# Kernel optimization log

Measured on AMD Instinct MI355X. Metric: run time of the kernel, lower is better.

The kernel has to match this reference:

```python
import jax, jax.numpy as jnp
import numpy as np


def setup_inputs() -> dict:
    key = jax.random.key(0)
    ks = jax.random.split(key, 9)
    B, Cin, H, W = 16, 512, 64, 64
    Cout = 256
    s_in = 0.02  # small init scale for stable softmax
    return {
        "x": jax.random.normal(ks[0], (B, Cin, H, W), dtype=jnp.float32),
        "Wq": jax.random.normal(ks[1], (Cout, Cin), dtype=jnp.float32) * s_in,
        "bq": jnp.zeros((Cout,), dtype=jnp.float32),
        "Wk": jax.random.normal(ks[2], (Cout, Cin), dtype=jnp.float32) * s_in,
        "bk": jnp.zeros((Cout,), dtype=jnp.float32),
        "Wv": jax.random.normal(ks[3], (Cout, Cin), dtype=jnp.float32) * s_in,
        "bv": jnp.zeros((Cout,), dtype=jnp.float32),
        "Wo": jax.random.normal(ks[4], (Cin, Cout), dtype=jnp.float32) * s_in,
        "bo": jnp.zeros((Cin,), dtype=jnp.float32),
    }


def reference(x, Wq, bq, Wk, bk, Wv, bv, Wo, bo):
    B, C, H, W = x.shape
    N = H * W
    xf = x.reshape(B, C, N)  # flatten spatial
    # 1x1 convs == per-pixel linear maps over channels
    q = jnp.einsum('oc,bcn->bon', Wq, xf) + bq[None, :, None]  # [B,Cout,N]
    k = jnp.einsum('oc,bcn->bon', Wk, xf) + bk[None, :, None]
    v = jnp.einsum('oc,bcn->bon', Wv, xf) + bv[None, :, None]
    # NOTE: original contracts over spatial dim N -> channel-attention [B,Cout,Cout]
    scale = jnp.asarray(N, x.dtype) ** 0.5  # query.size(-1) == N
    scores = jnp.einsum('bcn,bdn->bcd', q, k) / scale
    attn = jax.nn.softmax(scores, axis=-1)  # softmax over key-channel dim
    out = jnp.einsum('bcd,bdn->bcn', attn, v)  # [B,Cout,N]
    # permute(0,2,1).view(B,-1,H,W): row-major reshape of (B,N,Cout)
    out = jnp.transpose(out, (0, 2, 1)).reshape(B, -1, H, W)  # [B,Cout,H,W]
    out = jnp.einsum('co,bohw->bchw', Wo, out) + bo[None, :, None, None]
    return out
```

## Files before the change

kernel.cpp:

```cpp
#include <hip/hip_runtime.h>
#include <math.h>

typedef unsigned short u16;
typedef __bf16 bf16x8 __attribute__((ext_vector_type(8)));
typedef float f32x4 __attribute__((ext_vector_type(4)));
typedef unsigned short u16x4 __attribute__((ext_vector_type(4)));
typedef unsigned short u16x8 __attribute__((ext_vector_type(8)));

__device__ __forceinline__ u16 f2bf(float f) {
    unsigned int u = __float_as_uint(f);
    return (u16)((u + 0x7FFF + ((u >> 16) & 1)) >> 16);
}

#define BAR() do { __builtin_amdgcn_sched_barrier(0); __builtin_amdgcn_s_barrier(); __builtin_amdgcn_sched_barrier(0); } while (0)

__device__ __forceinline__ void stg(
    const u16* __restrict__ g, int ld, int row0, int rstride, int kt,
    u16* lds, int w, int l)
{
    #pragma unroll
    for (int qq = 0; qq < 2; ++qq) {
        const int c0 = qq * 512 + w * 64;
        const int c  = c0 + l;
        const int row = c >> 2, kcs = c & 3;
        const int kc  = kcs ^ ((row >> 1) & 3);
        const u16* src = g + (size_t)(row0 + row * rstride) * ld + kt + kc * 8;
        __builtin_amdgcn_global_load_lds(
            (const __attribute__((address_space(1))) unsigned int*)src,
            (__attribute__((address_space(3))) unsigned int*)(lds + (size_t)c0 * 8),
            16, 0, 0);
    }
}

template<int NT>
__device__ __forceinline__ void gemm256(
    const u16* __restrict__ Ag, int ldA, int baseA, int rsA,
    const u16* __restrict__ Bg, int ldB, int n0,
    u16* sm, f32x4 (&acc)[8][4])
{
    const int tid = threadIdx.x;
    const int l = tid & 63, w = tid >> 6;
    const int p = l & 15, g = l >> 4;
    const int wm = (w >> 2) * 128;
    const int wn = (w & 3) * 64;

    #pragma unroll
    for (int t = 0; t < 3; ++t) {
        u16* buf = sm + (t & 3) * 16384;
        stg(Ag, ldA, baseA, rsA, t * 32, buf, w, l);
        stg(Bg, ldB, n0, 1, t * 32, buf + 8192, w, l);
    }

    #pragma unroll
    for (int t = 0; t < NT; ++t) {
        u16* bufA = sm + (t & 3) * 16384;
        u16* bufB = bufA + 8192;
        u16* nbuf = sm + ((t + 3) & 3) * 16384;

        if (t + 3 < NT) stg(Ag, ldA, baseA, rsA, (t + 3) * 32, nbuf, w, l);
        {
            const int r = NT - 1 - t;
            if (r >= 3)      asm volatile("s_waitcnt vmcnt(10)" ::: "memory");
            else if (r == 2) asm volatile("s_waitcnt vmcnt(8)"  ::: "memory");
            else if (r == 1) asm volatile("s_waitcnt vmcnt(4)"  ::: "memory");
            else             asm volatile("s_waitcnt vmcnt(0)"  ::: "memory");
        }
        BAR();
        bf16x8 bfr[4];
        #pragma unroll
        for (int nf = 0; nf < 4; ++nf) {
            int row = wn + nf * 16 + p;
            bfr[nf] = *(const bf16x8*)(bufB + (size_t)(row * 4 + (g ^ ((row >> 1) & 3))) * 8);
        }
        {
            bf16x8 af[4];
            #pragma unroll
            for (int i = 0; i < 4; ++i) {
                int row = wm + i * 16 + p;
                af[i] = *(const bf16x8*)(bufA + (size_t)(row * 4 + (g ^ ((row >> 1) & 3))) * 8);
            }
            __builtin_amdgcn_s_setprio(1);
            #pragma unroll
            for (int i = 0; i < 4; ++i)
                #pragma unroll
                for (int nf = 0; nf < 4; ++nf)
                    acc[i][nf] = __builtin_amdgcn_mfma_f32_16x16x32_bf16(af[i], bfr[nf], acc[i][nf], 0, 0, 0);
            __builtin_amdgcn_s_setprio(0);
        }
        if (t + 3 < NT) stg(Bg, ldB, n0, 1, (t + 3) * 32, nbuf + 8192, w, l);
        {
            bf16x8 af[4];
            #pragma unroll
            for (int i = 0; i < 4; ++i) {
                int row = wm + (4 + i) * 16 + p;
                af[i] = *(const bf16x8*)(bufA + (size_t)(row * 4 + (g ^ ((row >> 1) & 3))) * 8);
            }
            __builtin_amdgcn_s_setprio(1);
            #pragma unroll
            for (int i = 0; i < 4; ++i)
                #pragma unroll
                for (int nf = 0; nf < 4; ++nf)
                    acc[4 + i][nf] = __builtin_amdgcn_mfma_f32_16x16x32_bf16(af[i], bfr[nf], acc[4 + i][nf], 0, 0, 0);
            __builtin_amdgcn_s_setprio(0);
        }
        BAR();
    }
}

__global__ __launch_bounds__(256) void k0_prep(
    const float* __restrict__ x, u16* __restrict__ xT,
    const float* __restrict__ Wq, const float* __restrict__ Wk,
    const float* __restrict__ Wv, const float* __restrict__ Wo,
    u16* __restrict__ wqk, u16* __restrict__ wv, u16* __restrict__ wo)
{
    const int tid = threadIdx.x;
    if (blockIdx.z == 16) {
        const int bid = blockIdx.y * 64 + blockIdx.x;
        const int sel = bid >> 7;
        const int sub = bid & 127;
        const float* s = sel == 0 ? Wq : sel == 1 ? Wk : sel == 2 ? Wv : Wo;
        u16* d = sel == 0 ? wqk : sel == 1 ? (wqk + 131072) : sel == 2 ? wv : wo;
        int i = (sub * 256 + tid) * 4;
        float4 v = *(const float4*)(s + i);
        u16x4 u = {f2bf(v.x), f2bf(v.y), f2bf(v.z), f2bf(v.w)};
        *(u16x4*)(d + i) = u;
        return;
    }
    __shared__ float Tx[64 * 65];
    const int b = blockIdx.z, c0 = blockIdx.y * 64, n0 = blockIdx.x * 64;
    const float* xb = x + (size_t)b * 512 * 4096;
    #pragma unroll
    for (int r = 0; r < 4; ++r) {
        int crow = (tid >> 4) + r * 16;
        int ncol = (tid & 15) * 4;
        float4 v = *(const float4*)(xb + (size_t)(c0 + crow) * 4096 + n0 + ncol);
        Tx[(ncol + 0) * 65 + crow] = v.x;
        Tx[(ncol + 1) * 65 + crow] = v.y;
        Tx[(ncol + 2) * 65 + crow] = v.z;
        Tx[(ncol + 3) * 65 + crow] = v.w;
    }
    __syncthreads();
    u16* ob = xT + (size_t)b * 4096 * 512;
    #pragma unroll
    for (int cc = 0; cc < 2; ++cc) {
        int id = cc * 256 + tid;
        int nrow = id >> 3;
        int cch = (id & 7) * 8;
        u16x8 u;
        #pragma unroll
        for (int j = 0; j < 8; ++j) u[j] = f2bf(Tx[nrow * 65 + cch + j]);
        *(u16x8*)(ob + (size_t)(n0 + nrow) * 512 + c0 + cch) = u;
    }
}

__global__ __launch_bounds__(512, 2) void k1_qkv(
    const u16* __restrict__ wqk, const u16* __restrict__ wv,
    const float* __restrict__ bq, const float* __restrict__ bk, const float* __restrict__ bv,
    const u16* __restrict__ xT, u16* __restrict__ q, u16* __restrict__ kmat,
    u16* __restrict__ vT)
{
    __shared__ u16 sm[65536];
    const int b = blockIdx.z;
    const int y = blockIdx.y;
    const u16* xb = xT + (size_t)b * 4096 * 512;

    const int tid = threadIdx.x;
    const int l = tid & 63, w = tid >> 6;
    const int p = l & 15, g = l >> 4;
    const int wm = (w >> 2) * 128, wn = (w & 3) * 64;

    f32x4 acc[8][4] = {};

    if (y < 2) {
        const int m0 = y * 256;
        const int n0 = blockIdx.x * 256;
        gemm256<16>(wqk, 512, m0, 1, xb, 512, n0, sm, acc);

        const float* bias = (y == 0) ? bq : bk;
        u16* outp = ((y == 0) ? q : kmat) + ((size_t)b << 20);
        #pragma unroll
        for (int mf = 0; mf < 8; ++mf)
            #pragma unroll
            for (int nf = 0; nf < 4; ++nf) {
                int n = n0 + wn + nf * 16 + p;
                #pragma unroll
                for (int r = 0; r < 4; ++r) {
                    int mloc = wm + mf * 16 + g * 4 + r;
                    outp[(size_t)mloc * 4096 + n] = f2bf(acc[mf][nf][r] + bias[mloc]);
                }
            }
    } else {
        const int m0 = blockIdx.x * 256;
        gemm256<16>(xb, 512, m0, 1, wv, 512, 0, sm, acc);

        u16* outp = vT + ((size_t)b << 20);
        #pragma unroll
        for (int nf = 0; nf < 4; ++nf) {
            int d = wn + nf * 16 + p;
            float bvv = bv[d];
            #pragma unroll
            for (int mf = 0; mf < 8; ++mf) {
                #pragma unroll
                for (int r = 0; r < 4; ++r) {
                    int row = m0 + wm + mf * 16 + g * 4 + r;
                    outp[(size_t)row * 256 + d] = f2bf(acc[mf][nf][r] + bvv);
                }
            }
        }
    }
}

__global__ __launch_bounds__(512, 2) void k2_scores(
    const u16* __restrict__ q, const u16* __restrict__ kmat, float* __restrict__ spart)
{
    __shared__ u16 sm[65536];
    const int b = blockIdx.z;
    const int split = blockIdx.x;
    const u16* A = q    + ((size_t)b << 20) + split * 512;
    const u16* B = kmat + ((size_t)b << 20) + split * 512;

    f32x4 acc[8][4] = {};
    gemm256<16>(A, 4096, 0, 1, B, 4096, 0, sm, acc);

    const int tid = threadIdx.x;
    const int l = tid & 63, w = tid >> 6;
    const int p = l & 15, g = l >> 4;
    const int wm = (w >> 2) * 128, wn = (w & 3) * 64;

    float* sp = spart + ((size_t)split * 16 + b) * 65536;
    #pragma unroll
    for (int mf = 0; mf < 8; ++mf)
        #pragma unroll
        for (int nf = 0; nf < 4; ++nf) {
            int n = wn + nf * 16 + p;
            #pragma unroll
            for (int r = 0; r < 4; ++r) {
                int m = wm + mf * 16 + g * 4 + r;
                sp[(size_t)m * 256 + n] = acc[mf][nf][r] * 0.015625f;
            }
        }
}

__global__ __launch_bounds__(256) void k3_softmax(
    const float* __restrict__ sp, u16* __restrict__ attn)
{
    const int row = blockIdx.x;
    const int tid = threadIdx.x;
    const size_t STRIDE = (size_t)16 * 65536;
    const size_t base = (size_t)row * 256 + tid;

    float s = 0.f;
    #pragma unroll
    for (int i = 0; i < 8; ++i) s += sp[base + i * STRIDE];

    __shared__ float red[4];
    float m = s;
    #pragma unroll
    for (int off = 32; off >= 1; off >>= 1) m = fmaxf(m, __shfl_xor(m, off));
    if ((tid & 63) == 0) red[tid >> 6] = m;
    __syncthreads();
    m = fmaxf(fmaxf(red[0], red[1]), fmaxf(red[2], red[3]));

    float e = expf(s - m);
    float t = e;
    #pragma unroll
    for (int off = 32; off >= 1; off >>= 1) t += __shfl_xor(t, off);
    __syncthreads();
    if ((tid & 63) == 0) red[tid >> 6] = t;
    __syncthreads();
    t = red[0] + red[1] + red[2] + red[3];

    attn[base] = f2bf(e / t);
}

__global__ __launch_bounds__(512, 2) void k4_pv(
    const u16* __restrict__ attn, const u16* __restrict__ vT, u16* __restrict__ outT3)
{
    __shared__ u16 sm[65536];
    const int b  = blockIdx.z;
    const int sh = blockIdx.x;
    const u16* A = vT   + ((size_t)b << 20);
    const u16* B = attn + ((size_t)b << 16);

    f32x4 acc[8][4] = {};
    gemm256<8>(A, 256, sh, 16, B, 256, 0, sm, acc);

    const int tid = threadIdx.x;
    const int l = tid & 63, w = tid >> 6;
    const int p = l & 15, g = l >> 4;
    const int wm = (w >> 2) * 128, wn = (w & 3) * 64;

    u16* outp = outT3 + (((size_t)b * 16 + sh) << 16);
    #pragma unroll
    for (int mf = 0; mf < 8; ++mf)
        #pragma unroll
        for (int nf = 0; nf < 4; ++nf) {
            int co  = wn + nf * 16 + p;
            int nh0 = wm + mf * 16 + g * 4;
            u16x4 u = {f2bf(acc[mf][nf][0]), f2bf(acc[mf][nf][1]),
                       f2bf(acc[mf][nf][2]), f2bf(acc[mf][nf][3])};
            *(u16x4*)(outp + (size_t)co * 256 + nh0) = u;
        }
}

__global__ __launch_bounds__(512, 2) void k5_final(
    const u16* __restrict__ wo, const float* __restrict__ bo,
    const u16* __restrict__ outT3, float* __restrict__ out)
{
    __shared__ u16 sm[65536];
    const int bz = blockIdx.z;
    const int b  = bz >> 4, sh = bz & 15;
    const int m0 = blockIdx.y * 256;
    const u16* B = outT3 + ((size_t)bz << 16);

    f32x4 acc[8][4] = {};
    gemm256<8>(wo, 256, m0, 1, B, 256, 0, sm, acc);

    const int tid = threadIdx.x;
    const int l = tid & 63, w = tid >> 6;
    const int p = l & 15, g = l >> 4;
    const int wm = (w >> 2) * 128, wn = (w & 3) * 64;

    float* ob = out + (size_t)b * 2097152 + (size_t)sh * 256;
    #pragma unroll
    for (int mf = 0; mf < 8; ++mf)
        #pragma unroll
        for (int nf = 0; nf < 4; ++nf) {
            int slo = wn + nf * 16 + p;
            #pragma unroll
            for (int r = 0; r < 4; ++r) {
                int m = m0 + wm + mf * 16 + g * 4 + r;
                ob[(size_t)m * 4096 + slo] = acc[mf][nf][r] + bo[m];
            }
        }
}

extern "C" void kernel_launch(void* const* d_in, const int* in_sizes, int n_in,
                              void* d_out, int out_size, void* d_ws, size_t ws_size,
                              hipStream_t stream) {
    (void)in_sizes; (void)n_in; (void)out_size; (void)ws_size;
    const float* x  = (const float*)d_in[0];
    const float* Wq = (const float*)d_in[1];
    const float* bq = (const float*)d_in[2];
    const float* Wk = (const float*)d_in[3];
    const float* bk = (const float*)d_in[4];
    const float* Wv = (const float*)d_in[5];
    const float* bv = (const float*)d_in[6];
    const float* Wo = (const float*)d_in[7];
    const float* bo = (const float*)d_in[8];
    float* out = (float*)d_out;

    char* ws = (char*)d_ws;
    u16* xT   = (u16*)(ws + 0);
    u16* q    = (u16*)(ws + 67108864);
    u16* kmat = (u16*)(ws + 100663296);
    u16* vT   = (u16*)(ws + 134217728);
    float* spart = (float*)(ws + 0);
    u16* attn    = (u16*)(ws + 67108864);
    u16* outT3   = (u16*)(ws + 100663296);
    u16* wqk  = (u16*)(ws + 167772160);
    u16* wv   = (u16*)(ws + 168296448);
    u16* wo   = (u16*)(ws + 168558592);

    k0_prep   <<<dim3(64, 8, 17), dim3(256), 0, stream>>>(x, xT, Wq, Wk, Wv, Wo, wqk, wv, wo);
    k1_qkv    <<<dim3(16, 3, 16), dim3(512), 0, stream>>>(wqk, wv, bq, bk, bv, xT, q, kmat, vT);
    k2_scores <<<dim3(8, 1, 16),  dim3(512), 0, stream>>>(q, kmat, spart);
    k3_softmax<<<dim3(4096),      dim3(256), 0, stream>>>(spart, attn);
    k4_pv     <<<dim3(16, 1, 16), dim3(512), 0, stream>>>(attn, vT, outT3);
    k5_final  <<<dim3(1, 2, 256), dim3(512), 0, stream>>>(wo, bo, outT3, out);
}
```

Before: 196.3 us.

## Shrink GEMM tiles to 256x128 with 4 waves and double buffering

The shared GEMM routine changes from a 256x256 tile with 8 waves and a 4-stage LDS pipeline to a 256x128 tile with 4 waves and a 2-stage double buffer. LDS drops to 48KB per block. The scores kernel splits K into 16 chunks instead of 8, so the softmax now sums 16 partials. Grids double so more blocks fill the CUs (3 per CU), at the cost of less operand reuse per block and a shallower prefetch.

```diff
diff --git a/kernel.cpp b/kernel.cpp
--- a/kernel.cpp
+++ b/kernel.cpp
@@ -14,13 +14,13 @@
 
 #define BAR() do { __builtin_amdgcn_sched_barrier(0); __builtin_amdgcn_s_barrier(); __builtin_amdgcn_sched_barrier(0); } while (0)
 
-__device__ __forceinline__ void stg(
+__device__ __forceinline__ void stgA(
     const u16* __restrict__ g, int ld, int row0, int rstride, int kt,
     u16* lds, int w, int l)
 {
     #pragma unroll
-    for (int qq = 0; qq < 2; ++qq) {
-        const int c0 = qq * 512 + w * 64;
+    for (int qq = 0; qq < 4; ++qq) {
+        const int c0 = qq * 256 + w * 64;
         const int c  = c0 + l;
         const int row = c >> 2, kcs = c & 3;
         const int kc  = kcs ^ ((row >> 1) & 3);
@@ -32,8 +32,26 @@
     }
 }
 
+__device__ __forceinline__ void stgB(
+    const u16* __restrict__ g, int ld, int n0, int kt,
+    u16* lds, int w, int l)
+{
+    #pragma unroll
+    for (int qq = 0; qq < 2; ++qq) {
+        const int c0 = qq * 256 + w * 64;
+        const int c  = c0 + l;
+        const int row = c >> 2, kcs = c & 3;
+        const int kc  = kcs ^ ((row >> 1) & 3);
+        const u16* src = g + (size_t)(n0 + row) * ld + kt + kc * 8;
+        __builtin_amdgcn_global_load_lds(
+            (const __attribute__((address_space(1))) unsigned int*)src,
+            (__attribute__((address_space(3))) unsigned int*)(lds + (size_t)c0 * 8),
+            16, 0, 0);
+    }
+}
+
 template<int NT>
-__device__ __forceinline__ void gemm256(
+__device__ __forceinline__ void gemmMN(
     const u16* __restrict__ Ag, int ldA, int baseA, int rsA,
     const u16* __restrict__ Bg, int ldB, int n0,
     u16* sm, f32x4 (&acc)[8][4])
@@ -41,29 +59,24 @@
     const int tid = threadIdx.x;
     const int l = tid & 63, w = tid >> 6;
     const int p = l & 15, g = l >> 4;
-    const int wm = (w >> 2) * 128;
-    const int wn = (w & 3) * 64;
-
-    #pragma unroll
-    for (int t = 0; t < 3; ++t) {
-        u16* buf = sm + (t & 3) * 16384;
-        stg(Ag, ldA, baseA, rsA, t * 32, buf, w, l);
-        stg(Bg, ldB, n0, 1, t * 32, buf + 8192, w, l);
-    }
+    const int wm = (w >> 1) * 128;
+    const int wn = (w & 1) * 64;
+
+    stgA(Ag, ldA, baseA, rsA, 0, sm, w, l);
+    stgB(Bg, ldB, n0, 0, sm + 8192, w, l);
 
     #pragma unroll
     for (int t = 0; t < NT; ++t) {
-        u16* bufA = sm + (t & 3) * 16384;
+        u16* bufA = sm + (t & 1) * 12288;
         u16* bufB = bufA + 8192;
-        u16* nbuf = sm + ((t + 3) & 3) * 16384;
-
-        if (t + 3 < NT) stg(Ag, ldA, baseA, rsA, (t + 3) * 32, nbuf, w, l);
-        {
-            const int r = NT - 1 - t;
-            if (r >= 3)      asm volatile("s_waitcnt vmcnt(10)" ::: "memory");
-            else if (r == 2) asm volatile("s_waitcnt vmcnt(8)"  ::: "memory");
-            else if (r == 1) asm volatile("s_waitcnt vmcnt(4)"  ::: "memory");
-            else             asm volatile("s_waitcnt vmcnt(0)"  ::: "memory");
+        u16* nbuf = sm + ((t + 1) & 1) * 12288;
+
+        if (t + 1 < NT) {
+            stgA(Ag, ldA, baseA, rsA, (t + 1) * 32, nbuf, w, l);
+            stgB(Bg, ldB, n0, (t + 1) * 32, nbuf + 8192, w, l);
+            asm volatile("s_waitcnt vmcnt(6)" ::: "memory");
+        } else {
+            asm volatile("s_waitcnt vmcnt(0)" ::: "memory");
         }
         BAR();
         bf16x8 bfr[4];
@@ -87,7 +100,6 @@
                     acc[i][nf] = __builtin_amdgcn_mfma_f32_16x16x32_bf16(af[i], bfr[nf], acc[i][nf], 0, 0, 0);
             __builtin_amdgcn_s_setprio(0);
         }
-        if (t + 3 < NT) stg(Bg, ldB, n0, 1, (t + 3) * 32, nbuf + 8192, w, l);
         {
             bf16x8 af[4];
             #pragma unroll
@@ -153,13 +165,13 @@
     }
 }
 
-__global__ __launch_bounds__(512, 2) void k1_qkv(
+__global__ __launch_bounds__(256, 3) void k1_qkv(
     const u16* __restrict__ wqk, const u16* __restrict__ wv,
     const float* __restrict__ bq, const float* __restrict__ bk, const float* __restrict__ bv,
     const u16* __restrict__ xT, u16* __restrict__ q, u16* __restrict__ kmat,
     u16* __restrict__ vT)
 {
-    __shared__ u16 sm[65536];
+    __shared__ u16 sm[24576];
     const int b = blockIdx.z;
     const int y = blockIdx.y;
     const u16* xb = xT + (size_t)b * 4096 * 512;
@@ -167,14 +179,14 @@
     const int tid = threadIdx.x;
     const int l = tid & 63, w = tid >> 6;
     const int p = l & 15, g = l >> 4;
-    const int wm = (w >> 2) * 128, wn = (w & 3) * 64;
+    const int wm = (w >> 1) * 128, wn = (w & 1) * 64;
 
     f32x4 acc[8][4] = {};
 
     if (y < 2) {
         const int m0 = y * 256;
-        const int n0 = blockIdx.x * 256;
-        gemm256<16>(wqk, 512, m0, 1, xb, 512, n0, sm, acc);
+        const int n0 = blockIdx.x * 128;
+        gemmMN<16>(wqk, 512, m0, 1, xb, 512, n0, sm, acc);
 
         const float* bias = (y == 0) ? bq : bk;
         u16* outp = ((y == 0) ? q : kmat) + ((size_t)b << 20);
@@ -190,13 +202,14 @@
                 }
             }
     } else {
-        const int m0 = blockIdx.x * 256;
-        gemm256<16>(xb, 512, m0, 1, wv, 512, 0, sm, acc);
+        const int m0 = (blockIdx.x >> 1) * 256;
+        const int n0 = (blockIdx.x & 1) * 128;
+        gemmMN<16>(xb, 512, m0, 1, wv, 512, n0, sm, acc);
 
         u16* outp = vT + ((size_t)b << 20);
         #pragma unroll
         for (int nf = 0; nf < 4; ++nf) {
-            int d = wn + nf * 16 + p;
+            int d = n0 + wn + nf * 16 + p;
             float bvv = bv[d];
             #pragma unroll
             for (int mf = 0; mf < 8; ++mf) {
@@ -210,29 +223,30 @@
     }
 }
 
-__global__ __launch_bounds__(512, 2) void k2_scores(
+__global__ __launch_bounds__(256, 3) void k2_scores(
     const u16* __restrict__ q, const u16* __restrict__ kmat, float* __restrict__ spart)
 {
-    __shared__ u16 sm[65536];
+    __shared__ u16 sm[24576];
     const int b = blockIdx.z;
-    const int split = blockIdx.x;
-    const u16* A = q    + ((size_t)b << 20) + split * 512;
-    const u16* B = kmat + ((size_t)b << 20) + split * 512;
+    const int split = blockIdx.x >> 1;
+    const int n0 = (blockIdx.x & 1) * 128;
+    const u16* A = q    + ((size_t)b << 20) + split * 256;
+    const u16* B = kmat + ((size_t)b << 20) + split * 256;
 
     f32x4 acc[8][4] = {};
-    gemm256<16>(A, 4096, 0, 1, B, 4096, 0, sm, acc);
-
-    const int tid = threadIdx.x;
-    const int l = tid & 63, w = tid >> 6;
-    const int p = l & 15, g = l >> 4;
-    const int wm = (w >> 2) * 128, wn = (w & 3) * 64;
+    gemmMN<8>(A, 4096, 0, 1, B, 4096, n0, sm, acc);
+
+    const int tid = threadIdx.x;
+    const int l = tid & 63, w = tid >> 6;
+    const int p = l & 15, g = l >> 4;
+    const int wm = (w >> 1) * 128, wn = (w & 1) * 64;
 
     float* sp = spart + ((size_t)split * 16 + b) * 65536;
     #pragma unroll
     for (int mf = 0; mf < 8; ++mf)
         #pragma unroll
         for (int nf = 0; nf < 4; ++nf) {
-            int n = wn + nf * 16 + p;
+            int n = n0 + wn + nf * 16 + p;
             #pragma unroll
             for (int r = 0; r < 4; ++r) {
                 int m = wm + mf * 16 + g * 4 + r;
@@ -251,7 +265,7 @@
 
     float s = 0.f;
     #pragma unroll
-    for (int i = 0; i < 8; ++i) s += sp[base + i * STRIDE];
+    for (int i = 0; i < 16; ++i) s += sp[base + i * STRIDE];
 
     __shared__ float red[4];
     float m = s;
@@ -273,29 +287,30 @@
     attn[base] = f2bf(e / t);
 }
 
-__global__ __launch_bounds__(512, 2) void k4_pv(
+__global__ __launch_bounds__(256, 3) void k4_pv(
     const u16* __restrict__ attn, const u16* __restrict__ vT, u16* __restrict__ outT3)
 {
-    __shared__ u16 sm[65536];
+    __shared__ u16 sm[24576];
     const int b  = blockIdx.z;
-    const int sh = blockIdx.x;
+    const int sh = blockIdx.x >> 1;
+    const int n0 = (blockIdx.x & 1) * 128;
     const u16* A = vT   + ((size_t)b << 20);
     const u16* B = attn + ((size_t)b << 16);
 
     f32x4 acc[8][4] = {};
-    gemm256<8>(A, 256, sh, 16, B, 256, 0, sm, acc);
-
-    const int tid = threadIdx.x;
-    const int l = tid & 63, w = tid >> 6;
-    const int p = l & 15, g = l >> 4;
-    const int wm = (w >> 2) * 128, wn = (w & 3) * 64;
+    gemmMN<8>(A, 256, sh, 16, B, 256, n0, sm, acc);
+
+    const int tid = threadIdx.x;
+    const int l = tid & 63, w = tid >> 6;
+    const int p = l & 15, g = l >> 4;
+    const int wm = (w >> 1) * 128, wn = (w & 1) * 64;
 
     u16* outp = outT3 + (((size_t)b * 16 + sh) << 16);
     #pragma unroll
     for (int mf = 0; mf < 8; ++mf)
         #pragma unroll
         for (int nf = 0; nf < 4; ++nf) {
-            int co  = wn + nf * 16 + p;
+            int co  = n0 + wn + nf * 16 + p;
             int nh0 = wm + mf * 16 + g * 4;
             u16x4 u = {f2bf(acc[mf][nf][0]), f2bf(acc[mf][nf][1]),
                        f2bf(acc[mf][nf][2]), f2bf(acc[mf][nf][3])};
@@ -303,30 +318,31 @@
         }
 }
 
-__global__ __launch_bounds__(512, 2) void k5_final(
+__global__ __launch_bounds__(256, 3) void k5_final(
     const u16* __restrict__ wo, const float* __restrict__ bo,
     const u16* __restrict__ outT3, float* __restrict__ out)
 {
-    __shared__ u16 sm[65536];
+    __shared__ u16 sm[24576];
     const int bz = blockIdx.z;
     const int b  = bz >> 4, sh = bz & 15;
-    const int m0 = blockIdx.y * 256;
+    const int m0 = (blockIdx.x & 1) * 256;
+    const int n0 = (blockIdx.x >> 1) * 128;
     const u16* B = outT3 + ((size_t)bz << 16);
 
     f32x4 acc[8][4] = {};
-    gemm256<8>(wo, 256, m0, 1, B, 256, 0, sm, acc);
-
-    const int tid = threadIdx.x;
-    const int l = tid & 63, w = tid >> 6;
-    const int p = l & 15, g = l >> 4;
-    const int wm = (w >> 2) * 128, wn = (w & 3) * 64;
+    gemmMN<8>(wo, 256, m0, 1, B, 256, n0, sm, acc);
+
+    const int tid = threadIdx.x;
+    const int l = tid & 63, w = tid >> 6;
+    const int p = l & 15, g = l >> 4;
+    const int wm = (w >> 1) * 128, wn = (w & 1) * 64;
 
     float* ob = out + (size_t)b * 2097152 + (size_t)sh * 256;
     #pragma unroll
     for (int mf = 0; mf < 8; ++mf)
         #pragma unroll
         for (int nf = 0; nf < 4; ++nf) {
-            int slo = wn + nf * 16 + p;
+            int slo = n0 + wn + nf * 16 + p;
             #pragma unroll
             for (int r = 0; r < 4; ++r) {
                 int m = m0 + wm + mf * 16 + g * 4 + r;
@@ -363,9 +379,9 @@
     u16* wo   = (u16*)(ws + 168558592);
 
     k0_prep   <<<dim3(64, 8, 17), dim3(256), 0, stream>>>(x, xT, Wq, Wk, Wv, Wo, wqk, wv, wo);
-    k1_qkv    <<<dim3(16, 3, 16), dim3(512), 0, stream>>>(wqk, wv, bq, bk, bv, xT, q, kmat, vT);
-    k2_scores <<<dim3(8, 1, 16),  dim3(512), 0, stream>>>(q, kmat, spart);
+    k1_qkv    <<<dim3(32, 3, 16), dim3(256), 0, stream>>>(wqk, wv, bq, bk, bv, xT, q, kmat, vT);
+    k2_scores <<<dim3(32, 1, 16), dim3(256), 0, stream>>>(q, kmat, spart);
     k3_softmax<<<dim3(4096),      dim3(256), 0, stream>>>(spart, attn);
-    k4_pv     <<<dim3(16, 1, 16), dim3(512), 0, stream>>>(attn, vT, outT3);
-    k5_final  <<<dim3(1, 2, 256), dim3(512), 0, stream>>>(wo, bo, outT3, out);
-}
+    k4_pv     <<<dim3(32, 1, 16), dim3(256), 0, stream>>>(attn, vT, outT3);
+    k5_final  <<<dim3(4, 1, 256), dim3(256), 0, stream>>>(wo, bo, outT3, out);
+}
```

New measurement: 368.9 us. +88.0%, slower.
